# Performance work log

Measured on AMD Instinct MI355X. Metric: run time of the kernel, lower is better.

The kernel has to match this reference:

```python
import jax, jax.numpy as jnp
import numpy as np

B, L, C, OUT = 8, 256, 512, 512


def setup_inputs() -> dict:
    key = jax.random.key(0)
    ks = jax.random.split(key, 8)
    xd = jax.random.normal(ks[0], (B, L, C), jnp.float32)
    xt = jax.random.normal(ks[1], (B, L, C), jnp.float32)
    # Linear weights stored (in, out): y = x @ W + b (equiv. to torch x @ W^T)
    Wc = jax.random.normal(ks[2], (C, C), jnp.float32) * 0.02
    bc = jnp.zeros((C,), jnp.float32)
    Wp = jax.random.normal(ks[3], (C, C), jnp.float32) * 0.02
    bp = jnp.zeros((C,), jnp.float32)
    Wf = jax.random.normal(ks[4], (C, OUT), jnp.float32) * 0.02
    bf = jnp.zeros((OUT,), jnp.float32)
    return {"xd": xd, "xt": xt, "Wc": Wc, "bc": bc, "Wp": Wp, "bp": bp, "Wf": Wf, "bf": bf}


def reference(xd, xt, Wc, bc, Wp, bp, Wf, bf):
    # projected features
    pt = jax.nn.relu(xt) @ Wp + bp              # (b, Lt, C)
    pc = jax.nn.relu(xd) @ Wc + bc              # (b, Ld, C)
    # sigmoid bilinear scores: (b, Lt, Ld) == (b, Ld, Lt) since Lt == Ld structurally
    scores = jax.nn.sigmoid(jnp.einsum('bic,bkc->bik', pt, pc))
    # normalize by total per-batch sum
    w = scores / jnp.sum(scores, axis=(1, 2), keepdims=True)
    # tanh of elementwise outer product, reduced with attention weights
    # cp[b,c] = sum_{i,j} tanh(xd[b,i,c] * xt[b,j,c]) * w[b,i,j]
    cp = jnp.einsum('bijc,bij->bc', jnp.tanh(xd[:, :, None, :] * xt[:, None, :, :]), w)
    return cp @ Wf + bf
```

## Files before the change

kernel.cpp:

```cpp
#include <hip/hip_runtime.h>
#include <math.h>

#define B_   8
#define L_   256
#define C_   512
#define OUT_ 512

typedef _Float16 half8 __attribute__((ext_vector_type(8)));
typedef float    f32x4 __attribute__((ext_vector_type(4)));

__global__ __launch_bounds__(256)
void wconv_kernel(const float* __restrict__ Wp, const float* __restrict__ Wc,
                  _Float16* __restrict__ hWp, _Float16* __restrict__ hWc)
{
    const int which = blockIdx.z;
    const float* __restrict__ W = which ? Wc : Wp;
    _Float16* __restrict__ H    = which ? hWc : hWp;
    __shared__ float tl[32][33];
    const int k0 = blockIdx.y << 5, n0 = blockIdx.x << 5;
    const int tr = threadIdx.x >> 5, tc = threadIdx.x & 31;
    #pragma unroll
    for (int i = 0; i < 32; i += 8)
        tl[tr + i][tc] = W[(size_t)(k0 + tr + i) * C_ + n0 + tc];
    __syncthreads();
    #pragma unroll
    for (int i = 0; i < 32; i += 8)
        H[(size_t)(n0 + tr + i) * C_ + k0 + tc] = (_Float16)tl[tc][tr + i];
}

__global__ __launch_bounds__(256)
void proj_mfma_kernel(const float* __restrict__ xt, const _Float16* __restrict__ hWp,
                      const float* __restrict__ bp,
                      const float* __restrict__ xd, const _Float16* __restrict__ hWc,
                      const float* __restrict__ bc,
                      _Float16* __restrict__ pt, _Float16* __restrict__ pc)
{
    const int which = blockIdx.z;
    const float*    __restrict__ X    = which ? xd : xt;
    const _Float16* __restrict__ W    = which ? hWc : hWp;
    const float*    __restrict__ bias = which ? bc : bp;
    _Float16*       __restrict__ Y    = which ? pc : pt;

    __shared__ _Float16 Ah[64][40];
    __shared__ _Float16 Bh[64][40];
    __shared__ _Float16 Ot[64][72];

    const int tid = threadIdx.x;
    const int m0 = blockIdx.y << 6, n0 = blockIdx.x << 6;
    const int srow = tid >> 2, sch = (tid & 3) << 3;
    const int lane = tid & 63, wv = tid >> 6;
    const int l15 = lane & 15, quad = lane >> 4;

    f32x4 acc[4] = {};
    const float*    Ag = X + (size_t)(m0 + srow) * C_ + sch;
    const _Float16* Bg = W + (size_t)(n0 + srow) * C_ + sch;

    for (int ks = 0; ks < 16; ++ks) {
        float4 a0 = *(const float4*)(Ag);
        float4 a1 = *(const float4*)(Ag + 4);
        half8 bv = *(const half8*)(Bg);
        Ag += 32; Bg += 32;
        half8 av;
        av[0] = (_Float16)fmaxf(a0.x, 0.f);
        av[1] = (_Float16)fmaxf(a0.y, 0.f);
        av[2] = (_Float16)fmaxf(a0.z, 0.f);
        av[3] = (_Float16)fmaxf(a0.w, 0.f);
        av[4] = (_Float16)fmaxf(a1.x, 0.f);
        av[5] = (_Float16)fmaxf(a1.y, 0.f);
        av[6] = (_Float16)fmaxf(a1.z, 0.f);
        av[7] = (_Float16)fmaxf(a1.w, 0.f);
        *(half8*)&Ah[srow][sch] = av;
        *(half8*)&Bh[srow][sch] = bv;
        __syncthreads();
        half8 af = *(const half8*)&Ah[(wv << 4) + l15][quad << 3];
        #pragma unroll
        for (int nb = 0; nb < 4; ++nb) {
            half8 bf = *(const half8*)&Bh[(nb << 4) + l15][quad << 3];
            acc[nb] = __builtin_amdgcn_mfma_f32_16x16x32_f16(af, bf, acc[nb], 0, 0, 0);
        }
        __syncthreads();
    }

    #pragma unroll
    for (int nb = 0; nb < 4; ++nb) {
        const float bz = bias[n0 + (nb << 4) + l15];
        #pragma unroll
        for (int r = 0; r < 4; ++r)
            Ot[(wv << 4) + (quad << 2) + r][(nb << 4) + l15] = (_Float16)(acc[nb][r] + bz);
    }
    __syncthreads();
    const int erow = tid >> 3, ech = (tid & 7) << 3;
    #pragma unroll
    for (int h = 0; h < 64; h += 32)
        *(half8*)&Y[(size_t)(m0 + erow + h) * C_ + n0 + ech] = *(const half8*)&Ot[erow + h][ech];
}

__global__ __launch_bounds__(256)
void sc_gemm_mfma_kernel(const _Float16* __restrict__ pt, const _Float16* __restrict__ pc,
                         float* __restrict__ dot0, float* __restrict__ dot1)
{
    const int b = blockIdx.z >> 1, ks = blockIdx.z & 1;
    const _Float16* __restrict__ A  = pt + (size_t)b * L_ * C_ + (ks << 8);
    const _Float16* __restrict__ Bm = pc + (size_t)b * L_ * C_ + (ks << 8);
    float* __restrict__ D = (ks ? dot1 : dot0) + (size_t)b * L_ * L_;

    __shared__ _Float16 Ah[64][40];
    __shared__ _Float16 Bh[64][40];

    const int tid = threadIdx.x;
    const int m0 = blockIdx.y << 6, n0 = blockIdx.x << 6;
    const int srow = tid >> 2, sch = (tid & 3) << 3;
    const int lane = tid & 63, wv = tid >> 6;
    const int l15 = lane & 15, quad = lane >> 4;

    f32x4 acc[4] = {};
    const _Float16* Ag = A  + (size_t)(m0 + srow) * C_ + sch;
    const _Float16* Bg = Bm + (size_t)(n0 + srow) * C_ + sch;

    for (int t = 0; t < 8; ++t) {
        half8 av = *(const half8*)Ag;
        half8 bv = *(const half8*)Bg;
        Ag += 32; Bg += 32;
        *(half8*)&Ah[srow][sch] = av;
        *(half8*)&Bh[srow][sch] = bv;
        __syncthreads();
        half8 af = *(const half8*)&Ah[(wv << 4) + l15][quad << 3];
        #pragma unroll
        for (int nb = 0; nb < 4; ++nb) {
            half8 bf = *(const half8*)&Bh[(nb << 4) + l15][quad << 3];
            acc[nb] = __builtin_amdgcn_mfma_f32_16x16x32_f16(af, bf, acc[nb], 0, 0, 0);
        }
        __syncthreads();
    }
    #pragma unroll
    for (int nb = 0; nb < 4; ++nb)
        #pragma unroll
        for (int r = 0; r < 4; ++r)
            D[(size_t)(m0 + (wv << 4) + (quad << 2) + r) * L_ + n0 + (nb << 4) + l15] = acc[nb][r];
}

__global__ __launch_bounds__(256)
void sc_finish_kernel(float* __restrict__ dot0, const float* __restrict__ dot1,
                      float* __restrict__ sums_part)
{
    __shared__ float red[256];
    const int bl = blockIdx.x;
    const int b  = bl >> 6;
    const size_t base = (size_t)b * (L_ * L_) + (size_t)((bl & 63) << 10) + ((size_t)threadIdx.x << 2);
    float4 d0 = *(const float4*)&dot0[base];
    float4 d1 = *(const float4*)&dot1[base];
    float4 s;
    s.x = 1.0f / (1.0f + expf(-(d0.x + d1.x)));
    s.y = 1.0f / (1.0f + expf(-(d0.y + d1.y)));
    s.z = 1.0f / (1.0f + expf(-(d0.z + d1.z)));
    s.w = 1.0f / (1.0f + expf(-(d0.w + d1.w)));
    *(float4*)&dot0[base] = s;
    red[threadIdx.x] = (s.x + s.y) + (s.z + s.w);
    __syncthreads();
    for (int st = 128; st > 0; st >>= 1) {
        if (threadIdx.x < st) red[threadIdx.x] += red[threadIdx.x + st];
        __syncthreads();
    }
    if (threadIdx.x == 0) sums_part[bl] = red[0];
}

__device__ __forceinline__ float sig2r(float a) {
    float e = __builtin_amdgcn_exp2f(a);
    return __builtin_amdgcn_rcpf(e + 1.0f);
}

__global__ __launch_bounds__(256, 4)
void cp_partial_kernel(const float* __restrict__ xd, const float* __restrict__ xt,
                       const float* __restrict__ scores, float* __restrict__ partials)
{
    const int i0  = blockIdx.x << 5;
    const int j0  = blockIdx.y << 4;
    const int b   = blockIdx.z >> 1;
    const int tid = threadIdx.x;
    const int c   = ((blockIdx.z & 1) << 8) | tid;

    __shared__ float ws_[16][36];
    __shared__ float red[256];

    const float* __restrict__ sb = scores + (size_t)b * L_ * L_;
    float wl = 0.f;
    {
        const int jj = tid & 15;
        const int ib = (tid >> 4) << 1;
        #pragma unroll
        for (int r = 0; r < 2; ++r) {
            const float v = sb[(size_t)(i0 + ib + r) * L_ + j0 + jj];
            ws_[jj][ib + r] = v;
            wl += v;
        }
    }
    red[tid] = wl;
    __syncthreads();
    for (int s = 128; s > 0; s >>= 1) {
        if (tid < s) red[tid] += red[tid + s];
        __syncthreads();
    }
    const float wsum = red[0];

    float xds[32], xtv[16];
    const float* __restrict__ xdb = xd + ((size_t)(b * L_ + i0)) * C_ + c;
    const float* __restrict__ xtb = xt + ((size_t)(b * L_ + j0)) * C_ + c;
    #pragma unroll
    for (int i = 0; i < 32; ++i)
        xds[i] = xdb[(size_t)i * C_] * 2.8853900817779268f;
    #pragma unroll
    for (int j = 0; j < 16; ++j)
        xtv[j] = xtb[(size_t)j * C_];

    float a0 = 0.f, a1 = 0.f, a2 = 0.f, a3 = 0.f;
    #pragma unroll 2
    for (int jj = 0; jj < 16; ++jj) {
        const float xv = xtv[jj];
        #pragma unroll
        for (int i = 0; i < 32; i += 4) {
            const float4 w4 = *(const float4*)&ws_[jj][i];
            a0 = fmaf(w4.x, sig2r(xds[i + 0] * xv), a0);
            a1 = fmaf(w4.y, sig2r(xds[i + 1] * xv), a1);
            a2 = fmaf(w4.z, sig2r(xds[i + 2] * xv), a2);
            a3 = fmaf(w4.w, sig2r(xds[i + 3] * xv), a3);
        }
    }
    const float partial = wsum - 2.0f * ((a0 + a1) + (a2 + a3));
    const int p = ((int)blockIdx.x << 4) | (int)blockIdx.y;
    partials[(size_t)((b << 7) | p) * C_ + c] = partial;
}

__global__ __launch_bounds__(512)
void finalize_kernel(const float* __restrict__ partials, const float* __restrict__ sums_part,
                     const float* __restrict__ Wf, const float* __restrict__ bfv,
                     float* __restrict__ out)
{
    const int b = blockIdx.y;
    const int t = threadIdx.x;
    __shared__ float cp[C_];
    __shared__ float red[512];
    __shared__ float sumsh;

    float s = 0.f;
    #pragma unroll
    for (int p = 0; p < 128; ++p)
        s += partials[(size_t)((b << 7) | p) * C_ + t];
    cp[t] = s;

    red[t] = (t < 64) ? sums_part[(b << 6) | t] : 0.f;
    __syncthreads();
    for (int st = 256; st > 0; st >>= 1) {
        if (t < st) red[t] += red[t + st];
        __syncthreads();
    }
    if (t == 0) sumsh = red[0];
    __syncthreads();

    const float inv = 1.0f / sumsh;
    const int o  = ((int)blockIdx.x << 6) | (t & 63);
    const int c0 = (t >> 6) << 6;
    float acc = 0.f;
    #pragma unroll 8
    for (int i = 0; i < 64; ++i) {
        const int cc = c0 + i;
        acc = fmaf(cp[cc], Wf[(size_t)cc * OUT_ + o], acc);
    }
    red[t] = acc;
    __syncthreads();
    if (t < 64) {
        float a = 0.f;
        #pragma unroll
        for (int g = 0; g < 8; ++g) a += red[(g << 6) | t];
        out[(size_t)b * OUT_ + o] = fmaf(a, inv, bfv[o]);
    }
}

extern "C" void kernel_launch(void* const* d_in, const int* in_sizes, int n_in,
                              void* d_out, int out_size, void* d_ws, size_t ws_size,
                              hipStream_t stream)
{
    const float* xd = (const float*)d_in[0];
    const float* xt = (const float*)d_in[1];
    const float* Wc = (const float*)d_in[2];
    const float* bc = (const float*)d_in[3];
    const float* Wp = (const float*)d_in[4];
    const float* bp = (const float*)d_in[5];
    const float* Wf = (const float*)d_in[6];
    const float* bf = (const float*)d_in[7];
    float* out = (float*)d_out;

    _Float16* hWp = (_Float16*)d_ws;
    _Float16* hWc = hWp + 262144;
    _Float16* pt  = hWc + 262144;
    _Float16* pc  = pt + 1048576;
    float* dot0      = (float*)(pc + 1048576);
    float* dot1      = dot0 + 524288;
    float* sums_part = dot1 + 524288;
    float* partials  = sums_part + 512;

    wconv_kernel<<<dim3(16, 16, 2), 256, 0, stream>>>(Wp, Wc, hWp, hWc);
    proj_mfma_kernel<<<dim3(8, 32, 2), 256, 0, stream>>>(xt, hWp, bp, xd, hWc, bc, pt, pc);
    sc_gemm_mfma_kernel<<<dim3(4, 4, 16), 256, 0, stream>>>(pt, pc, dot0, dot1);
    sc_finish_kernel<<<512, 256, 0, stream>>>(dot0, dot1, sums_part);
    cp_partial_kernel<<<dim3(8, 16, 16), 256, 0, stream>>>(xd, xt, dot0, partials);
    finalize_kernel<<<dim3(8, 8), 512, 0, stream>>>(partials, sums_part, Wf, bf, out);
}
```

Baseline: 156.3 us.

## Double-buffer GEMM tiles, split score GEMM K four ways, drop per-block weight reduction

```diff
diff --git a/kernel.cpp b/kernel.cpp
--- a/kernel.cpp
+++ b/kernel.cpp
@@ -41,8 +41,8 @@
     const float*    __restrict__ bias = which ? bc : bp;
     _Float16*       __restrict__ Y    = which ? pc : pt;
 
-    __shared__ _Float16 Ah[64][40];
-    __shared__ _Float16 Bh[64][40];
+    __shared__ _Float16 Ah[2][64][40];
+    __shared__ _Float16 Bh[2][64][40];
     __shared__ _Float16 Ot[64][72];
 
     const int tid = threadIdx.x;
@@ -51,36 +51,51 @@
     const int lane = tid & 63, wv = tid >> 6;
     const int l15 = lane & 15, quad = lane >> 4;
 
-    f32x4 acc[4] = {};
     const float*    Ag = X + (size_t)(m0 + srow) * C_ + sch;
     const _Float16* Bg = W + (size_t)(n0 + srow) * C_ + sch;
 
+    float4 a0 = *(const float4*)(Ag);
+    float4 a1 = *(const float4*)(Ag + 4);
+    half8  bv = *(const half8*)(Bg);
+
+    {
+        half8 av;
+        av[0] = (_Float16)fmaxf(a0.x, 0.f); av[1] = (_Float16)fmaxf(a0.y, 0.f);
+        av[2] = (_Float16)fmaxf(a0.z, 0.f); av[3] = (_Float16)fmaxf(a0.w, 0.f);
+        av[4] = (_Float16)fmaxf(a1.x, 0.f); av[5] = (_Float16)fmaxf(a1.y, 0.f);
+        av[6] = (_Float16)fmaxf(a1.z, 0.f); av[7] = (_Float16)fmaxf(a1.w, 0.f);
+        *(half8*)&Ah[0][srow][sch] = av;
+        *(half8*)&Bh[0][srow][sch] = bv;
+    }
+
+    f32x4 acc[4] = {};
     for (int ks = 0; ks < 16; ++ks) {
-        float4 a0 = *(const float4*)(Ag);
-        float4 a1 = *(const float4*)(Ag + 4);
-        half8 bv = *(const half8*)(Bg);
-        Ag += 32; Bg += 32;
-        half8 av;
-        av[0] = (_Float16)fmaxf(a0.x, 0.f);
-        av[1] = (_Float16)fmaxf(a0.y, 0.f);
-        av[2] = (_Float16)fmaxf(a0.z, 0.f);
-        av[3] = (_Float16)fmaxf(a0.w, 0.f);
-        av[4] = (_Float16)fmaxf(a1.x, 0.f);
-        av[5] = (_Float16)fmaxf(a1.y, 0.f);
-        av[6] = (_Float16)fmaxf(a1.z, 0.f);
-        av[7] = (_Float16)fmaxf(a1.w, 0.f);
-        *(half8*)&Ah[srow][sch] = av;
-        *(half8*)&Bh[srow][sch] = bv;
+        const int cur = ks & 1;
+        if (ks < 15) {
+            Ag += 32; Bg += 32;
+            a0 = *(const float4*)(Ag);
+            a1 = *(const float4*)(Ag + 4);
+            bv = *(const half8*)(Bg);
+        }
         __syncthreads();
-        half8 af = *(const half8*)&Ah[(wv << 4) + l15][quad << 3];
+        half8 af = *(const half8*)&Ah[cur][(wv << 4) + l15][quad << 3];
         #pragma unroll
         for (int nb = 0; nb < 4; ++nb) {
-            half8 bf = *(const half8*)&Bh[(nb << 4) + l15][quad << 3];
+            half8 bf = *(const half8*)&Bh[cur][(nb << 4) + l15][quad << 3];
             acc[nb] = __builtin_amdgcn_mfma_f32_16x16x32_f16(af, bf, acc[nb], 0, 0, 0);
         }
-        __syncthreads();
-    }
-
+        if (ks < 15) {
+            half8 av;
+            av[0] = (_Float16)fmaxf(a0.x, 0.f); av[1] = (_Float16)fmaxf(a0.y, 0.f);
+            av[2] = (_Float16)fmaxf(a0.z, 0.f); av[3] = (_Float16)fmaxf(a0.w, 0.f);
+            av[4] = (_Float16)fmaxf(a1.x, 0.f); av[5] = (_Float16)fmaxf(a1.y, 0.f);
+            av[6] = (_Float16)fmaxf(a1.z, 0.f); av[7] = (_Float16)fmaxf(a1.w, 0.f);
+            *(half8*)&Ah[cur ^ 1][srow][sch] = av;
+            *(half8*)&Bh[cur ^ 1][srow][sch] = bv;
+        }
+    }
+
+    __syncthreads();
     #pragma unroll
     for (int nb = 0; nb < 4; ++nb) {
         const float bz = bias[n0 + (nb << 4) + l15];
@@ -97,15 +112,15 @@
 
 __global__ __launch_bounds__(256)
 void sc_gemm_mfma_kernel(const _Float16* __restrict__ pt, const _Float16* __restrict__ pc,
-                         float* __restrict__ dot0, float* __restrict__ dot1)
-{
-    const int b = blockIdx.z >> 1, ks = blockIdx.z & 1;
-    const _Float16* __restrict__ A  = pt + (size_t)b * L_ * C_ + (ks << 8);
-    const _Float16* __restrict__ Bm = pc + (size_t)b * L_ * C_ + (ks << 8);
-    float* __restrict__ D = (ks ? dot1 : dot0) + (size_t)b * L_ * L_;
-
-    __shared__ _Float16 Ah[64][40];
-    __shared__ _Float16 Bh[64][40];
+                         float* __restrict__ dotb)
+{
+    const int b = blockIdx.z >> 2, ks4 = blockIdx.z & 3;
+    const _Float16* __restrict__ A  = pt + (size_t)b * L_ * C_ + (ks4 << 7);
+    const _Float16* __restrict__ Bm = pc + (size_t)b * L_ * C_ + (ks4 << 7);
+    float* __restrict__ D = dotb + (size_t)ks4 * (B_ * L_ * L_) + (size_t)b * (L_ * L_);
+
+    __shared__ _Float16 Ah[2][64][40];
+    __shared__ _Float16 Bh[2][64][40];
 
     const int tid = threadIdx.x;
     const int m0 = blockIdx.y << 6, n0 = blockIdx.x << 6;
@@ -113,24 +128,33 @@
     const int lane = tid & 63, wv = tid >> 6;
     const int l15 = lane & 15, quad = lane >> 4;
 
-    f32x4 acc[4] = {};
     const _Float16* Ag = A  + (size_t)(m0 + srow) * C_ + sch;
     const _Float16* Bg = Bm + (size_t)(n0 + srow) * C_ + sch;
 
-    for (int t = 0; t < 8; ++t) {
-        half8 av = *(const half8*)Ag;
-        half8 bv = *(const half8*)Bg;
-        Ag += 32; Bg += 32;
-        *(half8*)&Ah[srow][sch] = av;
-        *(half8*)&Bh[srow][sch] = bv;
+    half8 av = *(const half8*)Ag;
+    half8 bv = *(const half8*)Bg;
+    *(half8*)&Ah[0][srow][sch] = av;
+    *(half8*)&Bh[0][srow][sch] = bv;
+
+    f32x4 acc[4] = {};
+    for (int t = 0; t < 4; ++t) {
+        const int cur = t & 1;
+        if (t < 3) {
+            Ag += 32; Bg += 32;
+            av = *(const half8*)Ag;
+            bv = *(const half8*)Bg;
+        }
         __syncthreads();
-        half8 af = *(const half8*)&Ah[(wv << 4) + l15][quad << 3];
+        half8 af = *(const half8*)&Ah[cur][(wv << 4) + l15][quad << 3];
         #pragma unroll
         for (int nb = 0; nb < 4; ++nb) {
-            half8 bf = *(const half8*)&Bh[(nb << 4) + l15][quad << 3];
+            half8 bf = *(const half8*)&Bh[cur][(nb << 4) + l15][quad << 3];
             acc[nb] = __builtin_amdgcn_mfma_f32_16x16x32_f16(af, bf, acc[nb], 0, 0, 0);
         }
-        __syncthreads();
+        if (t < 3) {
+            *(half8*)&Ah[cur ^ 1][srow][sch] = av;
+            *(half8*)&Bh[cur ^ 1][srow][sch] = bv;
+        }
     }
     #pragma unroll
     for (int nb = 0; nb < 4; ++nb)
@@ -140,21 +164,24 @@
 }
 
 __global__ __launch_bounds__(256)
-void sc_finish_kernel(float* __restrict__ dot0, const float* __restrict__ dot1,
-                      float* __restrict__ sums_part)
+void sc_finish_kernel(float* __restrict__ dotb, float* __restrict__ sums_part)
 {
     __shared__ float red[256];
     const int bl = blockIdx.x;
     const int b  = bl >> 6;
-    const size_t base = (size_t)b * (L_ * L_) + (size_t)((bl & 63) << 10) + ((size_t)threadIdx.x << 2);
-    float4 d0 = *(const float4*)&dot0[base];
-    float4 d1 = *(const float4*)&dot1[base];
+    const size_t off = (size_t)b * (L_ * L_) + (size_t)((bl & 63) << 10) + ((size_t)threadIdx.x << 2);
+    float4 d = *(const float4*)&dotb[off];
+    #pragma unroll
+    for (int k = 1; k < 4; ++k) {
+        float4 e = *(const float4*)&dotb[(size_t)k * (B_ * L_ * L_) + off];
+        d.x += e.x; d.y += e.y; d.z += e.z; d.w += e.w;
+    }
     float4 s;
-    s.x = 1.0f / (1.0f + expf(-(d0.x + d1.x)));
-    s.y = 1.0f / (1.0f + expf(-(d0.y + d1.y)));
-    s.z = 1.0f / (1.0f + expf(-(d0.z + d1.z)));
-    s.w = 1.0f / (1.0f + expf(-(d0.w + d1.w)));
-    *(float4*)&dot0[base] = s;
+    s.x = 1.0f / (1.0f + expf(-d.x));
+    s.y = 1.0f / (1.0f + expf(-d.y));
+    s.z = 1.0f / (1.0f + expf(-d.z));
+    s.w = 1.0f / (1.0f + expf(-d.w));
+    *(float4*)&dotb[off] = s;
     red[threadIdx.x] = (s.x + s.y) + (s.z + s.w);
     __syncthreads();
     for (int st = 128; st > 0; st >>= 1) {
@@ -180,27 +207,15 @@
     const int c   = ((blockIdx.z & 1) << 8) | tid;
 
     __shared__ float ws_[16][36];
-    __shared__ float red[256];
 
     const float* __restrict__ sb = scores + (size_t)b * L_ * L_;
-    float wl = 0.f;
     {
         const int jj = tid & 15;
         const int ib = (tid >> 4) << 1;
         #pragma unroll
-        for (int r = 0; r < 2; ++r) {
-            const float v = sb[(size_t)(i0 + ib + r) * L_ + j0 + jj];
-            ws_[jj][ib + r] = v;
-            wl += v;
-        }
-    }
-    red[tid] = wl;
-    __syncthreads();
-    for (int s = 128; s > 0; s >>= 1) {
-        if (tid < s) red[tid] += red[tid + s];
-        __syncthreads();
-    }
-    const float wsum = red[0];
+        for (int r = 0; r < 2; ++r)
+            ws_[jj][ib + r] = sb[(size_t)(i0 + ib + r) * L_ + j0 + jj];
+    }
 
     float xds[32], xtv[16];
     const float* __restrict__ xdb = xd + ((size_t)(b * L_ + i0)) * C_ + c;
@@ -211,6 +226,7 @@
     #pragma unroll
     for (int j = 0; j < 16; ++j)
         xtv[j] = xtb[(size_t)j * C_];
+    __syncthreads();
 
     float a0 = 0.f, a1 = 0.f, a2 = 0.f, a3 = 0.f;
     #pragma unroll 2
@@ -225,9 +241,8 @@
             a3 = fmaf(w4.w, sig2r(xds[i + 3] * xv), a3);
         }
     }
-    const float partial = wsum - 2.0f * ((a0 + a1) + (a2 + a3));
     const int p = ((int)blockIdx.x << 4) | (int)blockIdx.y;
-    partials[(size_t)((b << 7) | p) * C_ + c] = partial;
+    partials[(size_t)((b << 7) | p) * C_ + c] = (a0 + a1) + (a2 + a3);
 }
 
 __global__ __launch_bounds__(512)
@@ -241,13 +256,13 @@
     __shared__ float red[512];
     __shared__ float sumsh;
 
+    red[t] = (t < 64) ? sums_part[(b << 6) | t] : 0.f;
+
     float s = 0.f;
     #pragma unroll
     for (int p = 0; p < 128; ++p)
         s += partials[(size_t)((b << 7) | p) * C_ + t];
-    cp[t] = s;
-
-    red[t] = (t < 64) ? sums_part[(b << 6) | t] : 0.f;
+
     __syncthreads();
     for (int st = 256; st > 0; st >>= 1) {
         if (t < st) red[t] += red[t + st];
@@ -256,7 +271,9 @@
     if (t == 0) sumsh = red[0];
     __syncthreads();
 
-    const float inv = 1.0f / sumsh;
+    cp[t] = 1.0f - 2.0f * s / sumsh;
+    __syncthreads();
+
     const int o  = ((int)blockIdx.x << 6) | (t & 63);
     const int c0 = (t >> 6) << 6;
     float acc = 0.f;
@@ -271,7 +288,7 @@
         float a = 0.f;
         #pragma unroll
         for (int g = 0; g < 8; ++g) a += red[(g << 6) | t];
-        out[(size_t)b * OUT_ + o] = fmaf(a, inv, bfv[o]);
+        out[(size_t)b * OUT_ + o] = a + bfv[o];
     }
 }
 
@@ -293,15 +310,14 @@
     _Float16* hWc = hWp + 262144;
     _Float16* pt  = hWc + 262144;
     _Float16* pc  = pt + 1048576;
-    float* dot0      = (float*)(pc + 1048576);
-    float* dot1      = dot0 + 524288;
-    float* sums_part = dot1 + 524288;
-    float* partials  = sums_part + 512;
+    float* dotb      = (float*)(pc + 1048576);
+    float* sums_part = dotb + 4 * (B_ * L_ * L_);
+    float* partials  = (float*)pt;
 
     wconv_kernel<<<dim3(16, 16, 2), 256, 0, stream>>>(Wp, Wc, hWp, hWc);
     proj_mfma_kernel<<<dim3(8, 32, 2), 256, 0, stream>>>(xt, hWp, bp, xd, hWc, bc, pt, pc);
-    sc_gemm_mfma_kernel<<<dim3(4, 4, 16), 256, 0, stream>>>(pt, pc, dot0, dot1);
-    sc_finish_kernel<<<512, 256, 0, stream>>>(dot0, dot1, sums_part);
-    cp_partial_kernel<<<dim3(8, 16, 16), 256, 0, stream>>>(xd, xt, dot0, partials);
+    sc_gemm_mfma_kernel<<<dim3(4, 4, 32), 256, 0, stream>>>(pt, pc, dotb);
+    sc_finish_kernel<<<512, 256, 0, stream>>>(dotb, sums_part);
+    cp_partial_kernel<<<dim3(8, 16, 16), 256, 0, stream>>>(xd, xt, dotb, partials);
     finalize_kernel<<<dim3(8, 8), 512, 0, stream>>>(partials, sums_part, Wf, bf, out);
 }
```

After: 153.9 us. No clear change (-1.6%).
